# Performance work log

Measured on AMD Instinct MI355X. Metric: run time of the kernel, lower is better.

Reference implementation:

```python
import jax, jax.numpy as jnp
import numpy as np

WS = 7        # window size
IMG = 56      # input resolution (H = W)
BATCH = 32    # image batch
DIM = 384
HEADS = 12
HEAD_DIM = DIM // HEADS
N = WS * WS                      # tokens per window = 49
NW = (IMG // WS) * (IMG // WS)   # windows per image = 64
B_ = BATCH * NW                  # 2048
TBL = (2 * WS - 1) ** 2          # 169


def _rel_index(ws):
    # standard Swin relative position index, values in [0, (2ws-1)^2)
    coords = np.stack(np.meshgrid(np.arange(ws), np.arange(ws), indexing='ij'))
    coords = coords.reshape(2, -1)                       # (2, N)
    rel = coords[:, :, None] - coords[:, None, :]        # (2, N, N)
    rel = rel.transpose(1, 2, 0).astype(np.int64).copy()
    rel[:, :, 0] += ws - 1
    rel[:, :, 1] += ws - 1
    rel[:, :, 0] *= 2 * ws - 1
    return rel.sum(-1)                                   # (N, N)


def _shift_mask(H, W, ws, shift):
    # shifted-window attention mask, (nW, N, N) with 0 / -100
    img = np.zeros((H, W))
    cnt = 0
    for hs in (slice(0, -ws), slice(-ws, -shift), slice(-shift, None)):
        for wsl in (slice(0, -ws), slice(-ws, -shift), slice(-shift, None)):
            img[hs, wsl] = cnt
            cnt += 1
    win = img.reshape(H // ws, ws, W // ws, ws).transpose(0, 2, 1, 3).reshape(-1, ws * ws)
    diff = win[:, None, :] - win[:, :, None]
    return np.where(diff != 0, -100.0, 0.0).astype(np.float32)


def setup_inputs() -> dict:
    key = jax.random.key(0)
    ks = jax.random.split(key, 7)
    s = 0.02
    return {
        'x': jax.random.normal(ks[0], (B_, N, DIM), jnp.float32),
        'mask': jnp.asarray(_shift_mask(IMG, IMG, WS, WS // 2)),
        'rpe_indices': jnp.asarray(_rel_index(WS)),
        'qkv_w': jax.random.normal(ks[1], (3 * DIM, DIM), jnp.float32) * s,
        'qkv_b': jnp.zeros((3 * DIM,), jnp.float32),
        'proj_w': jax.random.normal(ks[2], (DIM, DIM), jnp.float32) * s,
        'proj_b': jnp.zeros((DIM,), jnp.float32),
        'q_rpe': jax.random.normal(ks[3], (HEADS, HEAD_DIM, TBL), jnp.float32) * s,
        'k_rpe': jax.random.normal(ks[4], (HEADS, HEAD_DIM, TBL), jnp.float32) * s,
        'v_rpe': jax.random.normal(ks[5], (HEADS, TBL, HEAD_DIM), jnp.float32) * s,
    }


def reference(x, mask, rpe_indices, qkv_w, qkv_b, proj_w, proj_b, q_rpe, k_rpe, v_rpe):
    B, n, C = x.shape
    h, hd = q_rpe.shape[0], q_rpe.shape[1]
    scale = hd ** -0.5

    qkv = x @ qkv_w.T + qkv_b                                   # (B, N, 3C)
    qkv = qkv.reshape(B, n, 3, h, hd).transpose(2, 0, 3, 1, 4)   # (3, B, h, N, hd)
    q, k, v = qkv[0] * scale, qkv[1], qkv[2]

    attn = jnp.einsum('bhid,bhjd->bhij', q, k)                   # (B, h, N, N)

    # Contextual q/k bias. The torch code does b_q.flatten(2)[:, :, rpe_indices]
    # with rpe_indices in [0, TBL): gathering from the flattened (N*TBL) axis with
    # indices < TBL selects row 0 of the N axis, i.e. b_q[:, :, 0, rpe_indices].
    # We compute only that row, which is mathematically identical.
    bq0 = jnp.einsum('bhd,hdt->bht', q[:, :, 0], q_rpe)          # (B, h, TBL)
    bk0 = jnp.einsum('bhd,hdt->bht', k[:, :, 0], k_rpe)          # (B, h, TBL)
    attn = attn + (bq0 + bk0)[:, :, rpe_indices]                 # gather -> (B, h, N, N)

    nW = mask.shape[0]
    attn = attn.reshape(B // nW, nW, h, n, n) + mask[None, :, None]
    attn = jax.nn.softmax(attn.reshape(B, h, n, n), axis=-1)

    # contextual v bias: w = v_rpe[:, rpe_indices] -> (h, N, N, hd)
    w = v_rpe[:, rpe_indices.reshape(-1)].reshape(h, n, n, hd)
    r_v = jnp.einsum('bhij,hijd->bihd', attn, w).reshape(B, n, C)

    out = jnp.einsum('bhij,bhjd->bihd', attn, v).reshape(B, n, C) + r_v
    out = out @ proj_w.T + proj_b
    return out, attn
```

## Files before the change

### kernel.cpp

```cpp
#include <hip/hip_runtime.h>


typedef unsigned int u32;
typedef unsigned short u16;
typedef __attribute__((ext_vector_type(8))) short bf16x8;
typedef __attribute__((ext_vector_type(4))) float f32x4;
typedef float f4a __attribute__((ext_vector_type(4), aligned(4)));

#define SCALE 0.17677669529663687f

__device__ __forceinline__ u16 f2b(float f) {
  union { float f; u32 u; } c; c.f = f;
  u32 u = c.u;
  return (u16)((u + 0x7FFFu + ((u >> 16) & 1u)) >> 16);
}
__device__ __forceinline__ float b2f(u16 s) {
  union { float f; u32 u; } c; c.u = ((u32)s) << 16;
  return c.f;
}
__device__ __forceinline__ void async16(void* lds, const void* g) {
  __builtin_amdgcn_global_load_lds(
      (const __attribute__((address_space(1))) u32*)g,
      (__attribute__((address_space(3))) u32*)lds, 16, 0, 0);
}

__global__ __launch_bounds__(256) void k_cast(const float* __restrict__ s,
                                              u16* __restrict__ d, int n4) {
  int i = blockIdx.x * 256 + threadIdx.x;
  int str = gridDim.x * 256;
  for (; i < n4; i += str) {
    float4 v = ((const float4*)s)[i];
    ushort4 o;
    o.x = f2b(v.x); o.y = f2b(v.y); o.z = f2b(v.z); o.w = f2b(v.w);
    ((ushort4*)d)[i] = o;
  }
}

__global__ __launch_bounds__(256) void k_mbi(const float* __restrict__ mask,
                                             const int* __restrict__ idx,
                                             u16* __restrict__ mbi) {
  int i = blockIdx.x * 256 + threadIdx.x;
  if (i >= 64 * 2401) return;
  int p = i % 2401;
  mbi[i] = (u16)(idx[p] | ((mask[i] != 0.0f) ? 256 : 0));
}

__global__ __launch_bounds__(256) void k_qkv(
    const u16* __restrict__ A, const u16* __restrict__ Bw,
    const float* __restrict__ bias, u16* __restrict__ outq) {
  int bx0 = blockIdx.x;
  int bx = (bx0 & 7) * 882 + (bx0 >> 3);
  int mt = bx / 9, nt = bx - mt * 9;
  size_t m0 = (size_t)mt * 128;
  int n0 = nt * 128;
  int tid = threadIdx.x;
  int w = tid >> 6, l = tid & 63;
  int wm = w >> 1, wn = w & 1;
  int lr = l & 15, lg = l >> 4, lk8 = lg << 3;
  __shared__ u16 At[128 * 32];
  __shared__ u16 Bt[128 * 32];
  f32x4 acc[4][4] = {};
  int row = tid >> 2, c8 = (tid & 3) << 3;
  const u16* gA = A + (m0 + row) * 384 + c8;
  const u16* gA2 = A + (m0 + row + 64) * 384 + c8;
  const u16* gB = Bw + (size_t)(n0 + row) * 384 + c8;
  const u16* gB2 = Bw + (size_t)(n0 + row + 64) * 384 + c8;
  for (int ks = 0; ks < 12; ++ks) {
    int k0 = ks * 32;
    async16(At + tid * 8, gA + k0);
    async16(At + (256 + tid) * 8, gA2 + k0);
    async16(Bt + tid * 8, gB + k0);
    async16(Bt + (256 + tid) * 8, gB2 + k0);
    __syncthreads();
    bf16x8 af[4], bfr[4];
#pragma unroll
    for (int mi = 0; mi < 4; ++mi)
      af[mi] = *(const bf16x8*)&At[(wm * 64 + mi * 16 + lr) * 32 + lk8];
#pragma unroll
    for (int ni = 0; ni < 4; ++ni)
      bfr[ni] = *(const bf16x8*)&Bt[(wn * 64 + ni * 16 + lr) * 32 + lk8];
#pragma unroll
    for (int mi = 0; mi < 4; ++mi)
#pragma unroll
      for (int ni = 0; ni < 4; ++ni)
        acc[mi][ni] = __builtin_amdgcn_mfma_f32_16x16x32_bf16(af[mi], bfr[ni], acc[mi][ni], 0, 0, 0);
    __syncthreads();
  }
#pragma unroll
  for (int ni = 0; ni < 4; ++ni) {
    int cc = n0 + wn * 64 + ni * 16 + lr;
    float bv = bias[cc];
    float sc = (cc < 384) ? SCALE : 1.0f;
#pragma unroll
    for (int mi = 0; mi < 4; ++mi)
#pragma unroll
      for (int r = 0; r < 4; ++r) {
        size_t rr = m0 + wm * 64 + mi * 16 + lg * 4 + r;
        outq[rr * 1152 + cc] = f2b((acc[mi][ni][r] + bv) * sc);
      }
  }
}

__global__ __launch_bounds__(256) void k_bqk(
    const u16* __restrict__ qkv, const float* __restrict__ q_rpe,
    const float* __restrict__ k_rpe, float* __restrict__ bqk) {
  int bx = blockIdx.x;
  int mtile = bx / 12, h = bx % 12;
  int b0 = mtile * 64;
  int tid = threadIdx.x;
  int w = tid >> 6, l = tid & 63;
  int lr = l & 15, g = l >> 4;

  __shared__ __align__(16) u16 At[64 * 64];
  __shared__ __align__(16) u16 Bt[192 * 64];

  {
    int m = tid >> 2;
#pragma unroll
    for (int rnd = 0; rnd < 2; ++rnd) {
      int c = (tid & 3) + rnd * 4;
      const u16* src = qkv + (size_t)(b0 + m) * 56448 + h * 32 +
                       ((c < 4) ? c * 8 : 384 + (c - 4) * 8);
      bf16x8 v = *(const bf16x8*)src;
      int byte = (m * 128 + c * 16) ^ ((m & 7) << 4);
      *(bf16x8*)((char*)At + byte) = v;
    }
  }
  if (tid < 192) {
    int t = tid;
#pragma unroll
    for (int c = 0; c < 8; ++c) {
      u16 pk[8];
#pragma unroll
      for (int e = 0; e < 8; ++e) {
        int d = (c & 3) * 8 + e;
        float v = 0.f;
        if (t < 169)
          v = (c < 4) ? q_rpe[(h * 32 + d) * 169 + t]
                      : k_rpe[(h * 32 + d) * 169 + t];
        pk[e] = f2b(v);
      }
      int byte = (t * 128 + c * 16) ^ ((t & 7) << 4);
      *(bf16x8*)((char*)Bt + byte) = *(bf16x8*)pk;
    }
  }
  __syncthreads();

  f32x4 acc[12] = {};
  bf16x8 af[2];
#pragma unroll
  for (int ks = 0; ks < 2; ++ks) {
    int row = w * 16 + lr;
    af[ks] = *(const bf16x8*)((const char*)At +
              ((row * 128 + ks * 64 + g * 16) ^ ((row & 7) << 4)));
  }
#pragma unroll
  for (int nt = 0; nt < 12; ++nt) {
#pragma unroll
    for (int ks = 0; ks < 2; ++ks) {
      int t = nt * 16 + lr;
      bf16x8 bf = *(const bf16x8*)((const char*)Bt +
                   ((t * 128 + ks * 64 + g * 16) ^ ((t & 7) << 4)));
      acc[nt] = __builtin_amdgcn_mfma_f32_16x16x32_bf16(af[ks], bf, acc[nt], 0, 0, 0);
    }
  }
#pragma unroll
  for (int nt = 0; nt < 12; ++nt) {
    int t = nt * 16 + lr;
    if (t < 169) {
#pragma unroll
      for (int r = 0; r < 4; ++r) {
        int b = b0 + w * 16 + g * 4 + r;
        bqk[((size_t)b * 12 + h) * 169 + t] = acc[nt][r];
      }
    }
  }
}

__global__ __launch_bounds__(256) void k_attn(
    const u16* __restrict__ qkv, const float* __restrict__ bqkG,
    const u16* __restrict__ mbi,
    float* __restrict__ attn, u16* __restrict__ o1) {
  int blk0 = blockIdx.x;
  int blk = (blk0 & 7) * 768 + (blk0 >> 3);
  int b = blk / 3, hg = blk % 3;
  int tid = threadIdx.x, w = tid >> 6, l = tid & 63;
  int h = hg * 4 + w;
  int lr = l & 15, g = l >> 4;

  __shared__ __align__(16) char LDSR[32160];
  u16* mbiL = (u16*)LDSR;
  float* bqkL = (float*)(LDSR + 4832);
  char* Uw = LDSR + 7584 + w * 6144;
  u16* vw = (u16*)Uw;
  char* slab = Uw + 4096;
  float* aw = (float*)Uw;

  const u16* qbase = qkv + (size_t)b * 49 * 1152 + h * 32;
  const u16* kbase = qbase + 384;
  const u16* vbase = qbase + 768;

  {
    const u16* mrow = mbi + (size_t)(b & 63) * 2401;
    for (int p = tid; p < 2401; p += 256) mbiL[p] = mrow[p];
  }
#pragma unroll
  for (int p = 0; p < 4; ++p) {
    int j = p * 16 + (l >> 2);
    int jr = (j < 49) ? j : 48;
    async16(vw + p * 512 + l * 8, vbase + (size_t)jr * 1152 + (l & 3) * 8);
  }
  {
    const float* bg = bqkG + ((size_t)b * 12 + h) * 169;
#pragma unroll
    for (int t0 = 0; t0 < 192; t0 += 64) {
      int t = t0 + l;
      if (t < 169) bqkL[w * 172 + t] = bg[t];
    }
  }

  bf16x8 qf[4], kf[4];
#pragma unroll
  for (int t = 0; t < 4; ++t) {
    int qi = t * 16 + lr;
    int qir = (qi < 49) ? qi : 48;
    qf[t] = *(const bf16x8*)(qbase + (size_t)qir * 1152 + g * 8);
    kf[t] = *(const bf16x8*)(kbase + (size_t)qir * 1152 + g * 8);
  }

  f32x4 S[4][4] = {};
#pragma unroll
  for (int mt = 0; mt < 4; ++mt)
#pragma unroll
    for (int nt = 0; nt < 4; ++nt)
      S[mt][nt] = __builtin_amdgcn_mfma_f32_16x16x32_bf16(kf[mt], qf[nt], S[mt][nt], 0, 0, 0);

  __syncthreads();

#pragma unroll
  for (int nt = 0; nt < 4; ++nt) {
    int qi = nt * 16 + lr;
#pragma unroll
    for (int mt = 0; mt < 4; ++mt)
#pragma unroll
      for (int r = 0; r < 4; ++r) {
        int kj = mt * 16 + g * 4 + r;
        float s = S[mt][nt][r];
        if (qi < 49 && kj < 49) {
          u16 t = mbiL[qi * 49 + kj];
          s += bqkL[w * 172 + (t & 255)] - 100.f * (float)(t >> 8);
        } else {
          s = -1e9f;
        }
        S[mt][nt][r] = s;
      }
  }

  float rinv[4];
#pragma unroll
  for (int nt = 0; nt < 4; ++nt) {
    float m = -1e30f;
#pragma unroll
    for (int mt = 0; mt < 4; ++mt)
#pragma unroll
      for (int r = 0; r < 4; ++r) m = fmaxf(m, S[mt][nt][r]);
    m = fmaxf(m, __shfl_xor(m, 16, 64));
    m = fmaxf(m, __shfl_xor(m, 32, 64));
    float sum = 0.f;
#pragma unroll
    for (int mt = 0; mt < 4; ++mt)
#pragma unroll
      for (int r = 0; r < 4; ++r) {
        float e = __expf(S[mt][nt][r] - m);
        S[mt][nt][r] = e;
        sum += e;
      }
    sum += __shfl_xor(sum, 16, 64);
    sum += __shfl_xor(sum, 32, 64);
    rinv[nt] = 1.f / sum;
  }

  bf16x8 va[2][2];
#pragma unroll
  for (int ks = 0; ks < 2; ++ks)
#pragma unroll
    for (int mtd = 0; mtd < 2; ++mtd)
#pragma unroll
      for (int jj = 0; jj < 8; ++jj)
        va[ks][mtd][jj] = (short)vw[(ks * 32 + g * 8 + jj) * 32 + mtd * 16 + lr];

  f32x4 O[2][4] = {};
  int swz = (lr & 7) << 4;
#pragma unroll
  for (int nt = 0; nt < 4; ++nt) {
#pragma unroll
    for (int mt = 0; mt < 4; ++mt) {
      u32 w0 = (u32)f2b(S[mt][nt][0]) | ((u32)f2b(S[mt][nt][1]) << 16);
      u32 w1 = (u32)f2b(S[mt][nt][2]) | ((u32)f2b(S[mt][nt][3]) << 16);
      int off = (lr * 128 + mt * 32 + g * 8) ^ swz;
      uint2 pk = {w0, w1};
      *(uint2*)(slab + off) = pk;
    }
    bf16x8 pb0 = *(const bf16x8*)(slab + ((lr * 128 + g * 16) ^ swz));
    bf16x8 pb1 = *(const bf16x8*)(slab + ((lr * 128 + 64 + g * 16) ^ swz));
#pragma unroll
    for (int mtd = 0; mtd < 2; ++mtd) {
      O[mtd][nt] = __builtin_amdgcn_mfma_f32_16x16x32_bf16(va[0][mtd], pb0, O[mtd][nt], 0, 0, 0);
      O[mtd][nt] = __builtin_amdgcn_mfma_f32_16x16x32_bf16(va[1][mtd], pb1, O[mtd][nt], 0, 0, 0);
    }
  }

  {
    u16* ob = o1 + (size_t)b * 49 * 384 + h * 32;
#pragma unroll
    for (int nti = 0; nti < 4; ++nti) {
      int i = nti * 16 + lr;
      if (i < 49) {
        float riv = rinv[nti];
#pragma unroll
        for (int mtd = 0; mtd < 2; ++mtd) {
          u32 w0 = (u32)f2b(O[mtd][nti][0] * riv) | ((u32)f2b(O[mtd][nti][1] * riv) << 16);
          u32 w1 = (u32)f2b(O[mtd][nti][2] * riv) | ((u32)f2b(O[mtd][nti][3] * riv) << 16);
          uint2 pk = {w0, w1};
          *(uint2*)&ob[(size_t)i * 384 + mtd * 16 + g * 4] = pk;
        }
      }
    }
  }

  float* ao = attn + (size_t)(b * 12 + h) * 2401;
#pragma unroll
  for (int nt = 0; nt < 4; ++nt) {
    int qi = nt * 16 + lr;
    if (qi < 49) {
      float riv = rinv[nt];
#pragma unroll
      for (int mt = 0; mt < 4; ++mt)
#pragma unroll
        for (int r = 0; r < 4; ++r) {
          int kj = mt * 16 + g * 4 + r;
          if (kj < 49) aw[lr * 49 + kj] = S[mt][nt][r] * riv;
        }
    }
    asm volatile("s_waitcnt lgkmcnt(0)" ::: "memory");
    int lim = (nt < 3) ? 784 : 49;
#pragma unroll
    for (int it = 0; it < 13; ++it) {
      int p = l + it * 64;
      if (p < lim) ao[nt * 784 + p] = aw[p];
    }
  }
}

__global__ __launch_bounds__(256) void k_rv(
    const float* __restrict__ attn, const int* __restrict__ idx,
    const float* __restrict__ v_rpe, u16* __restrict__ o1) {
  int bx = blockIdx.x;
  int bc = bx & 7;
  int hi = bx >> 3;
  int i = hi % 49, h = hi / 49;
  int b0 = bc * 256;
  int tid = threadIdx.x;
  int w = tid >> 6, l = tid & 63;
  int lr = l & 15, g = l >> 4;

  __shared__ __align__(16) u16 wT[32 * 64];

  if (tid < 196) {
    int j = tid >> 2, d0 = (tid & 3) * 8;
    const float* vr = v_rpe + ((size_t)h * 169 + idx[i * 49 + j]) * 32 + d0;
    float4 a = *(const float4*)vr;
    float4 bvv = *(const float4*)(vr + 4);
    float el[8] = {a.x, a.y, a.z, a.w, bvv.x, bvv.y, bvv.z, bvv.w};
#pragma unroll
    for (int e = 0; e < 8; ++e) {
      int d = d0 + e;
      int byte = (d * 128 + j * 2) ^ ((d & 7) << 4);
      *(u16*)((char*)wT + byte) = f2b(el[e]);
    }
  } else {
    int t = tid - 196;
    int j = 49 + (t >> 2), d0 = (t & 3) * 8;
#pragma unroll
    for (int e = 0; e < 8; ++e) {
      int d = d0 + e;
      int byte = (d * 128 + j * 2) ^ ((d & 7) << 4);
      *(u16*)((char*)wT + byte) = 0;
    }
  }
  __syncthreads();

  f32x4 acc[2][4] = {};
#pragma unroll
  for (int ks = 0; ks < 2; ++ks) {
    bf16x8 af[2];
#pragma unroll
    for (int mt = 0; mt < 2; ++mt) {
      int d = mt * 16 + lr;
      int byte = (d * 128 + ks * 64 + g * 16) ^ ((d & 7) << 4);
      af[mt] = *(const bf16x8*)((const char*)wT + byte);
    }
    int j0 = ks * 32 + g * 8;
#pragma unroll
    for (int nt = 0; nt < 4; ++nt) {
      int bl = w * 64 + nt * 16 + lr;
      const float* ar = attn + ((size_t)(b0 + bl) * 12 + h) * 2401 +
                        (size_t)i * 49 + j0;
      f4a v0 = *(const f4a*)ar;
      f4a v1 = *(const f4a*)(ar + 4);
      u16 pk[8];
#pragma unroll
      for (int e = 0; e < 8; ++e) {
        float vv = (e < 4) ? v0[e] : v1[e - 4];
        pk[e] = (j0 + e < 49) ? f2b(vv) : (u16)0;
      }
      bf16x8 bfr = *(bf16x8*)pk;
#pragma unroll
      for (int mt = 0; mt < 2; ++mt)
        acc[mt][nt] = __builtin_amdgcn_mfma_f32_16x16x32_bf16(af[mt], bfr, acc[mt][nt], 0, 0, 0);
    }
  }

#pragma unroll
  for (int nt = 0; nt < 4; ++nt) {
    int bl = w * 64 + nt * 16 + lr;
    u16* ob = o1 + ((size_t)(b0 + bl) * 49 + i) * 384 + h * 32;
#pragma unroll
    for (int mt = 0; mt < 2; ++mt) {
      int d = mt * 16 + g * 4;
      uint2 old = *(uint2*)&ob[d];
      uint2 nw;
      nw.x = (u32)f2b(b2f((u16)(old.x & 0xffff)) + acc[mt][nt][0]) |
             ((u32)f2b(b2f((u16)(old.x >> 16)) + acc[mt][nt][1]) << 16);
      nw.y = (u32)f2b(b2f((u16)(old.y & 0xffff)) + acc[mt][nt][2]) |
             ((u32)f2b(b2f((u16)(old.y >> 16)) + acc[mt][nt][3]) << 16);
      *(uint2*)&ob[d] = nw;
    }
  }
}

__global__ __launch_bounds__(256) void k_proj(
    const u16* __restrict__ A, const u16* __restrict__ Bw,
    const float* __restrict__ bias, float* __restrict__ out) {
  int bx0 = blockIdx.x;
  int bx = (bx0 & 7) * 294 + (bx0 >> 3);
  int mt = bx / 3, nt = bx - mt * 3;
  size_t m0 = (size_t)mt * 128;
  int n0 = nt * 128;
  int tid = threadIdx.x;
  int w = tid >> 6, l = tid & 63;
  int wm = w >> 1, wn = w & 1;
  int lr = l & 15, lg = l >> 4, lk8 = lg << 3;
  __shared__ u16 At[128 * 32];
  __shared__ u16 Bt[128 * 32];
  f32x4 acc[4][4] = {};
  int row = tid >> 2, c8 = (tid & 3) << 3;
  const u16* gA = A + (m0 + row) * 384 + c8;
  const u16* gA2 = A + (m0 + row + 64) * 384 + c8;
  const u16* gB = Bw + (size_t)(n0 + row) * 384 + c8;
  const u16* gB2 = Bw + (size_t)(n0 + row + 64) * 384 + c8;
  for (int ks = 0; ks < 12; ++ks) {
    int k0 = ks * 32;
    async16(At + tid * 8, gA + k0);
    async16(At + (256 + tid) * 8, gA2 + k0);
    async16(Bt + tid * 8, gB + k0);
    async16(Bt + (256 + tid) * 8, gB2 + k0);
    __syncthreads();
    bf16x8 af[4], bfr[4];
#pragma unroll
    for (int mi = 0; mi < 4; ++mi)
      af[mi] = *(const bf16x8*)&At[(wm * 64 + mi * 16 + lr) * 32 + lk8];
#pragma unroll
    for (int ni = 0; ni < 4; ++ni)
      bfr[ni] = *(const bf16x8*)&Bt[(wn * 64 + ni * 16 + lr) * 32 + lk8];
#pragma unroll
    for (int mi = 0; mi < 4; ++mi)
#pragma unroll
      for (int ni = 0; ni < 4; ++ni)
        acc[mi][ni] = __builtin_amdgcn_mfma_f32_16x16x32_bf16(af[mi], bfr[ni], acc[mi][ni], 0, 0, 0);
    __syncthreads();
  }
#pragma unroll
  for (int mi = 0; mi < 4; ++mi)
#pragma unroll
    for (int ni = 0; ni < 4; ++ni)
#pragma unroll
      for (int r = 0; r < 4; ++r) {
        int rr = wm * 64 + mi * 16 + lg * 4 + r;
        int cc = wn * 64 + ni * 16 + lr;
        out[(m0 + rr) * 384 + (size_t)(n0 + cc)] = acc[mi][ni][r] + bias[n0 + cc];
      }
}

extern "C" void kernel_launch(void* const* d_in, const int* in_sizes, int n_in,
                              void* d_out, int out_size, void* d_ws, size_t ws_size,
                              hipStream_t stream) {
  const float* x      = (const float*)d_in[0];
  const float* mask   = (const float*)d_in[1];
  const int*   rpe    = (const int*)d_in[2];
  const float* qkv_w  = (const float*)d_in[3];
  const float* qkv_b  = (const float*)d_in[4];
  const float* proj_w = (const float*)d_in[5];
  const float* proj_b = (const float*)d_in[6];
  const float* q_rpe  = (const float*)d_in[7];
  const float* k_rpe  = (const float*)d_in[8];
  const float* v_rpe  = (const float*)d_in[9];

  float* out  = (float*)d_out;
  float* attn = out + (size_t)100352 * 384;

  char* ws = (char*)d_ws;
  u16*   qkvb   = (u16*)ws;
  u16*   wqkvb  = (u16*)(ws + 231211008);
  u16*   wprojb = (u16*)(ws + 232095744);
  u16*   mbi    = (u16*)(ws + 232390656);
  float* bqkG   = (float*)(ws + 232697984);
  u16*   xb     = (u16*)(ws + 249311360);
  u16*   o1     = xb;

  k_cast<<<2048, 256, 0, stream>>>(x, xb, 9633792);
  k_cast<<<432, 256, 0, stream>>>(qkv_w, wqkvb, 110592);
  k_cast<<<144, 256, 0, stream>>>(proj_w, wprojb, 36864);
  k_mbi<<<601, 256, 0, stream>>>(mask, rpe, mbi);
  k_qkv<<<7056, 256, 0, stream>>>(xb, wqkvb, qkv_b, qkvb);
  k_bqk<<<384, 256, 0, stream>>>(qkvb, q_rpe, k_rpe, bqkG);
  k_attn<<<6144, 256, 0, stream>>>(qkvb, bqkG, mbi, attn, o1);
  k_rv<<<4704, 256, 0, stream>>>(attn, rpe, v_rpe, o1);
  k_proj<<<2352, 256, 0, stream>>>(o1, wprojb, proj_b, out);
}
```

Measured before the change: 583.7 us.

## Fuse x cast into QKV GEMM, merge prep kernels, double-buffer GEMM LDS

The QKV GEMM now reads fp32 x directly, converts it to bf16 in registers and stores it to LDS, which removes the separate cast pass over the large activation tensor and its bf16 round trip. The weight casts and the mask/index pack are merged into one prep launch. Both the QKV and projection GEMMs get double-buffered LDS with a one-step prefetch and explicit waitcnt/barrier control. Extra lgkmcnt waits are added in the attention store path. The risks are higher LDS and register use per block and the reliance on hand-written vmcnt counts being correct.

After: 599.2 us. 1.03x slower.

```diff
diff --git a/kernel.cpp b/kernel.cpp
--- a/kernel.cpp
+++ b/kernel.cpp
@@ -18,35 +18,41 @@
   union { float f; u32 u; } c; c.u = ((u32)s) << 16;
   return c.f;
 }
+__device__ __forceinline__ u32 pk2(float lo, float hi) {
+  return (u32)f2b(lo) | ((u32)f2b(hi) << 16);
+}
 __device__ __forceinline__ void async16(void* lds, const void* g) {
   __builtin_amdgcn_global_load_lds(
       (const __attribute__((address_space(1))) u32*)g,
       (__attribute__((address_space(3))) u32*)lds, 16, 0, 0);
 }
 
-__global__ __launch_bounds__(256) void k_cast(const float* __restrict__ s,
-                                              u16* __restrict__ d, int n4) {
-  int i = blockIdx.x * 256 + threadIdx.x;
-  int str = gridDim.x * 256;
-  for (; i < n4; i += str) {
-    float4 v = ((const float4*)s)[i];
-    ushort4 o;
-    o.x = f2b(v.x); o.y = f2b(v.y); o.z = f2b(v.z); o.w = f2b(v.w);
-    ((ushort4*)d)[i] = o;
-  }
-}
-
-__global__ __launch_bounds__(256) void k_mbi(const float* __restrict__ mask,
-                                             const int* __restrict__ idx,
-                                             u16* __restrict__ mbi) {
-  int i = blockIdx.x * 256 + threadIdx.x;
-  if (i >= 64 * 2401) return;
-  int p = i % 2401;
-  mbi[i] = (u16)(idx[p] | ((mask[i] != 0.0f) ? 256 : 0));
+__global__ __launch_bounds__(256) void k_prep(
+    const float* __restrict__ qkv_w, const float* __restrict__ proj_w,
+    const float* __restrict__ mask, const int* __restrict__ idx,
+    u16* __restrict__ wqkvb, u16* __restrict__ wprojb, u16* __restrict__ mbi) {
+  int bx = blockIdx.x, tid = threadIdx.x;
+  if (bx < 432) {
+    int i = bx * 256 + tid;
+    float4 v = ((const float4*)qkv_w)[i];
+    ushort4 o; o.x = f2b(v.x); o.y = f2b(v.y); o.z = f2b(v.z); o.w = f2b(v.w);
+    ((ushort4*)wqkvb)[i] = o;
+  } else if (bx < 576) {
+    int i = (bx - 432) * 256 + tid;
+    float4 v = ((const float4*)proj_w)[i];
+    ushort4 o; o.x = f2b(v.x); o.y = f2b(v.y); o.z = f2b(v.z); o.w = f2b(v.w);
+    ((ushort4*)wprojb)[i] = o;
+  } else {
+    int i = (bx - 576) * 256 + tid;
+    if (i < 64 * 2401) {
+      int p = i % 2401;
+      mbi[i] = (u16)(idx[p] | ((mask[i] != 0.0f) ? 256 : 0));
+    }
+  }
 }
 
 __global__ __launch_bounds__(256) void k_qkv(
-    const u16* __restrict__ A, const u16* __restrict__ Bw,
+    const float* __restrict__ X, const u16* __restrict__ Bw,
     const float* __restrict__ bias, u16* __restrict__ outq) {
   int bx0 = blockIdx.x;
   int bx = (bx0 & 7) * 882 + (bx0 >> 3);
@@ -57,34 +63,61 @@
   int w = tid >> 6, l = tid & 63;
   int wm = w >> 1, wn = w & 1;
   int lr = l & 15, lg = l >> 4, lk8 = lg << 3;
-  __shared__ u16 At[128 * 32];
-  __shared__ u16 Bt[128 * 32];
+
+  __shared__ u16 At[4096];
+  __shared__ u16 Bt[2][4096];
+
   f32x4 acc[4][4] = {};
   int row = tid >> 2, c8 = (tid & 3) << 3;
-  const u16* gA = A + (m0 + row) * 384 + c8;
-  const u16* gA2 = A + (m0 + row + 64) * 384 + c8;
-  const u16* gB = Bw + (size_t)(n0 + row) * 384 + c8;
+  const u16* gB  = Bw + (size_t)(n0 + row) * 384 + c8;
   const u16* gB2 = Bw + (size_t)(n0 + row + 64) * 384 + c8;
-  for (int ks = 0; ks < 12; ++ks) {
-    int k0 = ks * 32;
-    async16(At + tid * 8, gA + k0);
-    async16(At + (256 + tid) * 8, gA2 + k0);
-    async16(Bt + tid * 8, gB + k0);
-    async16(Bt + (256 + tid) * 8, gB2 + k0);
-    __syncthreads();
+  const float* gX  = X + (m0 + row) * 384 + c8;
+  const float* gX2 = X + (m0 + row + 64) * 384 + c8;
+
+  float4 ar[2][4];
+  async16(&Bt[0][tid * 8], gB);
+  async16(&Bt[0][(256 + tid) * 8], gB2);
+  ar[0][0] = *(const float4*)(gX);
+  ar[0][1] = *(const float4*)(gX + 4);
+  ar[0][2] = *(const float4*)(gX2);
+  ar[0][3] = *(const float4*)(gX2 + 4);
+
+#pragma unroll
+  for (int t = 0; t < 12; ++t) {
+    int cur = t & 1, nxt = cur ^ 1;
+    int k1 = ((t < 11) ? (t + 1) : 11) * 32;
+    async16(&Bt[nxt][tid * 8], gB + k1);
+    async16(&Bt[nxt][(256 + tid) * 8], gB2 + k1);
+    ar[nxt][0] = *(const float4*)(gX + k1);
+    ar[nxt][1] = *(const float4*)(gX + k1 + 4);
+    ar[nxt][2] = *(const float4*)(gX2 + k1);
+    ar[nxt][3] = *(const float4*)(gX2 + k1 + 4);
+    asm volatile("s_waitcnt vmcnt(6)" ::: "memory");
+    u32 p0[4], p1[4];
+    p0[0] = pk2(ar[cur][0].x, ar[cur][0].y);
+    p0[1] = pk2(ar[cur][0].z, ar[cur][0].w);
+    p0[2] = pk2(ar[cur][1].x, ar[cur][1].y);
+    p0[3] = pk2(ar[cur][1].z, ar[cur][1].w);
+    p1[0] = pk2(ar[cur][2].x, ar[cur][2].y);
+    p1[1] = pk2(ar[cur][2].z, ar[cur][2].w);
+    p1[2] = pk2(ar[cur][3].x, ar[cur][3].y);
+    p1[3] = pk2(ar[cur][3].z, ar[cur][3].w);
+    *(uint4*)&At[tid * 8] = *(uint4*)p0;
+    *(uint4*)&At[(256 + tid) * 8] = *(uint4*)p1;
+    asm volatile("s_waitcnt lgkmcnt(0)\n\ts_barrier" ::: "memory");
     bf16x8 af[4], bfr[4];
 #pragma unroll
     for (int mi = 0; mi < 4; ++mi)
       af[mi] = *(const bf16x8*)&At[(wm * 64 + mi * 16 + lr) * 32 + lk8];
 #pragma unroll
     for (int ni = 0; ni < 4; ++ni)
-      bfr[ni] = *(const bf16x8*)&Bt[(wn * 64 + ni * 16 + lr) * 32 + lk8];
+      bfr[ni] = *(const bf16x8*)&Bt[cur][(wn * 64 + ni * 16 + lr) * 32 + lk8];
 #pragma unroll
     for (int mi = 0; mi < 4; ++mi)
 #pragma unroll
       for (int ni = 0; ni < 4; ++ni)
         acc[mi][ni] = __builtin_amdgcn_mfma_f32_16x16x32_bf16(af[mi], bfr[ni], acc[mi][ni], 0, 0, 0);
-    __syncthreads();
+    asm volatile("s_waitcnt lgkmcnt(0)\n\ts_barrier" ::: "memory");
   }
 #pragma unroll
   for (int ni = 0; ni < 4; ++ni) {
@@ -328,6 +361,7 @@
     }
   }
 
+  asm volatile("s_waitcnt lgkmcnt(0)" ::: "memory");
   float* ao = attn + (size_t)(b * 12 + h) * 2401;
 #pragma unroll
   for (int nt = 0; nt < 4; ++nt) {
@@ -349,6 +383,7 @@
       int p = l + it * 64;
       if (p < lim) ao[nt * 784 + p] = aw[p];
     }
+    asm volatile("s_waitcnt lgkmcnt(0)" ::: "memory");
   }
 }
 
@@ -451,34 +486,45 @@
   int w = tid >> 6, l = tid & 63;
   int wm = w >> 1, wn = w & 1;
   int lr = l & 15, lg = l >> 4, lk8 = lg << 3;
-  __shared__ u16 At[128 * 32];
-  __shared__ u16 Bt[128 * 32];
+
+  __shared__ u16 At[2][4096];
+  __shared__ u16 Bt[2][4096];
+
   f32x4 acc[4][4] = {};
   int row = tid >> 2, c8 = (tid & 3) << 3;
-  const u16* gA = A + (m0 + row) * 384 + c8;
+  const u16* gA  = A + (m0 + row) * 384 + c8;
   const u16* gA2 = A + (m0 + row + 64) * 384 + c8;
-  const u16* gB = Bw + (size_t)(n0 + row) * 384 + c8;
+  const u16* gB  = Bw + (size_t)(n0 + row) * 384 + c8;
   const u16* gB2 = Bw + (size_t)(n0 + row + 64) * 384 + c8;
-  for (int ks = 0; ks < 12; ++ks) {
-    int k0 = ks * 32;
-    async16(At + tid * 8, gA + k0);
-    async16(At + (256 + tid) * 8, gA2 + k0);
-    async16(Bt + tid * 8, gB + k0);
-    async16(Bt + (256 + tid) * 8, gB2 + k0);
-    __syncthreads();
+
+  async16(&At[0][tid * 8], gA);
+  async16(&At[0][(256 + tid) * 8], gA2);
+  async16(&Bt[0][tid * 8], gB);
+  async16(&Bt[0][(256 + tid) * 8], gB2);
+
+#pragma unroll
+  for (int t = 0; t < 12; ++t) {
+    int cur = t & 1, nxt = cur ^ 1;
+    int k1 = ((t < 11) ? (t + 1) : 11) * 32;
+    async16(&At[nxt][tid * 8], gA + k1);
+    async16(&At[nxt][(256 + tid) * 8], gA2 + k1);
+    async16(&Bt[nxt][tid * 8], gB + k1);
+    async16(&Bt[nxt][(256 + tid) * 8], gB2 + k1);
+    asm volatile("s_waitcnt vmcnt(4)" ::: "memory");
+    asm volatile("s_barrier" ::: "memory");
     bf16x8 af[4], bfr[4];
 #pragma unroll
     for (int mi = 0; mi < 4; ++mi)
-      af[mi] = *(const bf16x8*)&At[(wm * 64 + mi * 16 + lr) * 32 + lk8];
+      af[mi] = *(const bf16x8*)&At[cur][(wm * 64 + mi * 16 + lr) * 32 + lk8];
 #pragma unroll
     for (int ni = 0; ni < 4; ++ni)
-      bfr[ni] = *(const bf16x8*)&Bt[(wn * 64 + ni * 16 + lr) * 32 + lk8];
+      bfr[ni] = *(const bf16x8*)&Bt[cur][(wn * 64 + ni * 16 + lr) * 32 + lk8];
 #pragma unroll
     for (int mi = 0; mi < 4; ++mi)
 #pragma unroll
       for (int ni = 0; ni < 4; ++ni)
         acc[mi][ni] = __builtin_amdgcn_mfma_f32_16x16x32_bf16(af[mi], bfr[ni], acc[mi][ni], 0, 0, 0);
-    __syncthreads();
+    asm volatile("s_waitcnt lgkmcnt(0)\n\ts_barrier" ::: "memory");
   }
 #pragma unroll
   for (int mi = 0; mi < 4; ++mi)
@@ -515,14 +561,10 @@
   u16*   wprojb = (u16*)(ws + 232095744);
   u16*   mbi    = (u16*)(ws + 232390656);
   float* bqkG   = (float*)(ws + 232697984);
-  u16*   xb     = (u16*)(ws + 249311360);
-  u16*   o1     = xb;
-
-  k_cast<<<2048, 256, 0, stream>>>(x, xb, 9633792);
-  k_cast<<<432, 256, 0, stream>>>(qkv_w, wqkvb, 110592);
-  k_cast<<<144, 256, 0, stream>>>(proj_w, wprojb, 36864);
-  k_mbi<<<601, 256, 0, stream>>>(mask, rpe, mbi);
-  k_qkv<<<7056, 256, 0, stream>>>(xb, wqkvb, qkv_b, qkvb);
+  u16*   o1     = (u16*)(ws + 249311360);
+
+  k_prep<<<1177, 256, 0, stream>>>(qkv_w, proj_w, mask, rpe, wqkvb, wprojb, mbi);
+  k_qkv<<<7056, 256, 0, stream>>>(x, wqkvb, qkv_b, qkvb);
   k_bqk<<<384, 256, 0, stream>>>(qkvb, q_rpe, k_rpe, bqkG);
   k_attn<<<6144, 256, 0, stream>>>(qkvb, bqkG, mbi, attn, o1);
   k_rv<<<4704, 256, 0, stream>>>(attn, rpe, v_rpe, o1);
```
